# Kernel tuning notes

Hardware: AMD Instinct MI355X
Metric: run time of the kernel (lower is better)

Reference implementation:

```python
import jax, jax.numpy as jnp
import numpy as np

B, S, D, H, F, M, DC = 2, 1024, 1024, 16, 4096, 2048, 256
HD = D // H

def rmsnorm(x, w, eps=1e-6):
    return x * jax.lax.rsqrt(jnp.mean(x * x, axis=-1, keepdims=True) + eps) * w

def setup_inputs() -> dict:
    key = jax.random.key(0)
    ks = jax.random.split(key, 16)
    def w(i, shape):
        return jax.random.normal(ks[i], shape, jnp.float32) * (1.0 / np.sqrt(shape[0]))
    # real RoPE tables
    inv = 1.0 / (10000.0 ** (jnp.arange(0, HD, 2, dtype=jnp.float32) / HD))
    freqs = jnp.outer(jnp.arange(S, dtype=jnp.float32), inv)
    emb = jnp.concatenate([freqs, freqs], axis=-1)  # [S, HD]
    return {
        "hidden_states": jax.random.normal(ks[0], (B, S, D), jnp.float32),
        "mem_keys": jnp.zeros((B, M, DC), jnp.float32),
        "mem_values": jnp.zeros((B, M, D), jnp.float32),
        "cos": jnp.cos(emb), "sin": jnp.sin(emb),
        "norm1_w": jnp.ones((D,), jnp.float32),
        "norm2_w": jnp.ones((D,), jnp.float32),
        "norm_mem_w": jnp.ones((D,), jnp.float32),
        "Wq": w(1, (D, D)), "Wk": w(2, (D, D)), "Wv": w(3, (D, D)), "Wo": w(4, (D, D)),
        "W_content": w(5, (D, D)), "W_comp": w(6, (D, DC)), "W_strength": w(7, (D, 1)),
        "W_query": w(8, (D, DC)),
        "W_gate": w(9, (2 * D, D)), "W_proj": w(10, (D, D)),
        "W1": w(11, (D, F)), "W3": w(12, (D, F)), "W2": w(13, (F, D)),
        "position": 0,
    }

def reference(hidden_states, mem_keys, mem_values, cos, sin,
              norm1_w, norm2_w, norm_mem_w,
              Wq, Wk, Wv, Wo,
              W_content, W_comp, W_strength, W_query,
              W_gate, W_proj, W1, W3, W2, position):
    b, s, d = hidden_states.shape
    h = hidden_states
    # 1) causal self-attention with RoPE
    n = rmsnorm(h, norm1_w)
    def heads(x):
        return x.reshape(b, s, H, HD).transpose(0, 2, 1, 3)  # [b,h,s,hd]
    q, k, v = heads(n @ Wq), heads(n @ Wk), heads(n @ Wv)
    def rot(x):
        x1, x2 = jnp.split(x, 2, axis=-1)
        return jnp.concatenate([-x2, x1], axis=-1)
    c, si = cos[None, None], sin[None, None]
    q = q * c + rot(q) * si
    k = k * c + rot(k) * si
    scores = jnp.einsum('bhqd,bhkd->bhqk', q, k) / np.sqrt(HD)
    causal = jnp.tril(jnp.ones((s, s), bool))
    scores = jnp.where(causal, scores, jnp.float32(-1e30))
    attn = jax.nn.softmax(scores, axis=-1)
    attn_out = jnp.einsum('bhqk,bhkd->bhqd', attn, v).transpose(0, 2, 1, 3).reshape(b, s, d) @ Wo
    h = h + attn_out
    # 2) memory snapshot write: the original per-token python loop writes each token
    #    to consecutive circular-buffer slots; with M >= s the slots are unique, so
    #    the loop vectorizes into a single scatter.
    content = h @ W_content                     # [b,s,d]
    compressed = h @ W_comp                     # [b,s,DC]
    strength = jax.nn.sigmoid(h @ W_strength)   # [b,s,1]
    idx = (position + jnp.arange(s)) % mem_keys.shape[1]
    old_k = mem_keys[:, idx]
    old_v = mem_values[:, idx]
    new_keys = mem_keys.at[:, idx].set(strength * compressed + (1.0 - strength) * old_k)
    new_values = mem_values.at[:, idx].set(strength * content + (1.0 - strength) * old_v)
    # 3) memory retrieval (attention over slots)
    normed = rmsnorm(h, norm_mem_w)
    qm = normed @ W_query                       # [b,s,DC]
    mscores = jnp.einsum('bsd,bmd->bsm', qm, new_keys) / np.sqrt(DC)
    mattn = jax.nn.softmax(mscores, axis=-1)
    retrieved = jnp.einsum('bsm,bmd->bsd', mattn, new_values)
    # 4) gated memory integration
    gate = jax.nn.sigmoid(jnp.concatenate([h, retrieved], axis=-1) @ W_gate)
    h = h + gate * (retrieved @ W_proj)
    # 5) SwiGLU FFN
    n2 = rmsnorm(h, norm2_w)
    h = h + (jax.nn.silu(n2 @ W1) * (n2 @ W3)) @ W2
    return (h, new_keys, new_values)
```

## Files before the change

kernel.cpp:

```cpp
#include <hip/hip_runtime.h>
#include <hip/hip_bf16.h>
#include <math.h>

typedef __bf16 bf16;
typedef __attribute__((ext_vector_type(8))) __bf16 bf16x8;
typedef __attribute__((ext_vector_type(4))) __bf16 bf16x4;
typedef __attribute__((ext_vector_type(4))) float f32x4;

#define B_ 2
#define S_ 1024
#define D_ 1024
#define H_ 16
#define HD_ 64
#define F_ 4096
#define M_ 2048
#define DC_ 256
#define NTOK (B_*S_)

__device__ __forceinline__ void gload16(const void* g, void* l) {
    __builtin_amdgcn_global_load_lds(
        (__attribute__((address_space(1))) void*)(void*)(g),
        (__attribute__((address_space(3))) void*)(l), 16, 0, 0);
}

template<int N> __device__ __forceinline__ void wait_vm() {
    if constexpr (N == 0)      asm volatile("s_waitcnt vmcnt(0)" ::: "memory");
    else if constexpr (N == 2) asm volatile("s_waitcnt vmcnt(2)" ::: "memory");
    else if constexpr (N == 4) asm volatile("s_waitcnt vmcnt(4)" ::: "memory");
    else if constexpr (N == 6) asm volatile("s_waitcnt vmcnt(6)" ::: "memory");
    else                       asm volatile("s_waitcnt vmcnt(8)" ::: "memory");
}
__device__ __forceinline__ void wait_lgkm0() {
    asm volatile("s_waitcnt lgkmcnt(0)" ::: "memory");
}
__device__ __forceinline__ float sigm(float x) { return 1.f / (1.f + expf(-x)); }

template<int BM, int BN, bool OUTBF, int EPI>
__global__ __launch_bounds__(256) void mgemm(
    const bf16* __restrict__ A, const bf16* __restrict__ Bt,
    const float* __restrict__ resid, void* __restrict__ Cout,
    int K, int lda, int ldb, int ldc,
    long long sA, long long sB, long long sC,
    const void* __restrict__ aux1, const void* __restrict__ aux2)
{
    constexpr int WN   = (BM == 128) ? 2 : 4;
    constexpr int WCOL = BN / WN;
    constexpr int FN   = WCOL / 16;
    constexpr int LA = BM * 64, LB = BN * 64;
    constexpr int LPS = BM / 32 + BN / 32;
    __shared__ bf16 lds[2 * (LA + LB)];
    const int z = blockIdx.z;
    A  += (size_t)z * sA;
    Bt += (size_t)z * sB;
    const int gx = gridDim.x;
    const int nwg = gx * gridDim.y;
    const int flat = blockIdx.y * gx + blockIdx.x;
    const int q8 = nwg >> 3, r8 = nwg & 7;
    const int xcd = flat & 7, lid = flat >> 3;
    const int swz = (xcd < r8 ? xcd * (q8 + 1) : r8 * (q8 + 1) + (xcd - r8) * q8) + lid;
    const int band = swz / (8 * gx);
    const int rem  = swz % (8 * gx);
    const int row0 = (band * 8 + (rem & 7)) * BM;
    const int col0 = (rem >> 3) * BN;
    const int tid = threadIdx.x, wid = tid >> 6, lane = tid & 63;
    const int wr = wid / WN, wc = wid % WN;
    const int srow = lane >> 3;
    const int ssub = (lane & 7) ^ (srow & 7);

    f32x4 acc[4][FN];
    #pragma unroll
    for (int m = 0; m < 4; ++m)
        #pragma unroll
        for (int n = 0; n < FN; ++n) acc[m][n] = (f32x4){0.f, 0.f, 0.f, 0.f};

    auto STAGE = [&](int buf, int k0) {
        bf16* Ab = lds + buf * (LA + LB);
        bf16* Bb = Ab + LA;
        #pragma unroll
        for (int i = 0; i < BM / 32; ++i) {
            int c = wid * (BM / 32) + i;
            gload16(A + (size_t)(row0 + c * 8 + srow) * lda + k0 + ssub * 8, Ab + c * 512);
        }
        #pragma unroll
        for (int i = 0; i < BN / 32; ++i) {
            int c = wid * (BN / 32) + i;
            gload16(Bt + (size_t)(col0 + c * 8 + srow) * ldb + k0 + ssub * 8, Bb + c * 512);
        }
    };

    const int nt = K >> 6;
    STAGE(0, 0);
    if (nt > 1) STAGE(1, 64);
    for (int t = 0; t < nt; ++t) {
        if (t < nt - 1) wait_vm<LPS>();
        else            wait_vm<0>();
        __builtin_amdgcn_sched_barrier(0);
        __builtin_amdgcn_s_barrier();
        __builtin_amdgcn_sched_barrier(0);
        const bf16* Ab = lds + (t & 1) * (LA + LB);
        const bf16* Bb = Ab + LA;
        const int ar = wr * 64 + (lane & 15);
        const int br = wc * WCOL + (lane & 15);
        #pragma unroll
        for (int ksel = 0; ksel < 2; ++ksel) {
            const int ps = ((ksel << 2) + (lane >> 4)) ^ (lane & 7);
            bf16x8 af[4], bfr[FN];
            #pragma unroll
            for (int m = 0; m < 4; ++m)
                af[m] = *(const bf16x8*)(Ab + (ar + m * 16) * 64 + ps * 8);
            #pragma unroll
            for (int n = 0; n < FN; ++n)
                bfr[n] = *(const bf16x8*)(Bb + (br + n * 16) * 64 + ps * 8);
            #pragma unroll
            for (int m = 0; m < 4; ++m)
                #pragma unroll
                for (int n = 0; n < FN; ++n)
                    acc[m][n] = __builtin_amdgcn_mfma_f32_16x16x32_bf16(af[m], bfr[n], acc[m][n], 0, 0, 0);
        }
        wait_lgkm0();
        __builtin_amdgcn_sched_barrier(0);
        __builtin_amdgcn_s_barrier();
        __builtin_amdgcn_sched_barrier(0);
        if (t + 2 < nt) STAGE(t & 1, (t + 2) << 6);
    }
    const int crow = row0 + wr * 64 + ((lane >> 4) << 2);
    const int ccol = col0 + wc * WCOL + (lane & 15);
    #pragma unroll
    for (int m = 0; m < 4; ++m)
        #pragma unroll
        for (int n = 0; n < FN; ++n)
            #pragma unroll
            for (int r = 0; r < 4; ++r) {
                const int rr = crow + m * 16 + r, cc = ccol + n * 16;
                size_t idx = (size_t)rr * ldc + cc;
                float v = acc[m][n][r];
                if (EPI == 2) {
                    float g = sigm((float)((const bf16*)aux1)[idx]);
                    v = ((const float*)aux2)[idx] + g * v;
                    ((float*)Cout)[idx] = v;
                } else {
                    if (resid) v += resid[idx];
                    if (OUTBF) ((bf16*)Cout)[(size_t)z * sC + idx] = (bf16)v;
                    else       ((float*)Cout)[(size_t)z * sC + idx] = v;
                    if (EPI == 1)
                        ((bf16*)aux1)[(size_t)rr * 2048 + cc] = (bf16)v;
                }
            }
}

__global__ __launch_bounds__(256) void mgemm13(
    const bf16* __restrict__ A, const bf16* __restrict__ B1t, const bf16* __restrict__ B3t,
    bf16* __restrict__ Cout, int K, int lda, int ldb, int ldc)
{
    constexpr int LA = 128 * 64, LB = 64 * 64;
    __shared__ bf16 lds[2 * (LA + 2 * LB)];
    const int gx = gridDim.x;
    const int nwg = gx * gridDim.y;
    const int flat = blockIdx.y * gx + blockIdx.x;
    const int q8 = nwg >> 3, r8 = nwg & 7;
    const int xcd = flat & 7, lid = flat >> 3;
    const int swz = (xcd < r8 ? xcd * (q8 + 1) : r8 * (q8 + 1) + (xcd - r8) * q8) + lid;
    const int band = swz / (8 * gx);
    const int rem  = swz % (8 * gx);
    const int row0 = (band * 8 + (rem & 7)) * 128;
    const int col0 = (rem >> 3) * 64;
    const int tid = threadIdx.x, wid = tid >> 6, lane = tid & 63;
    const int wr = wid >> 1, wc = wid & 1;
    const int srow = lane >> 3;
    const int ssub = (lane & 7) ^ (srow & 7);

    f32x4 acc1[4][2], acc3[4][2];
    #pragma unroll
    for (int m = 0; m < 4; ++m)
        #pragma unroll
        for (int n = 0; n < 2; ++n) {
            acc1[m][n] = (f32x4){0.f, 0.f, 0.f, 0.f};
            acc3[m][n] = (f32x4){0.f, 0.f, 0.f, 0.f};
        }

    auto STAGE = [&](int buf, int k0) {
        bf16* Ab = lds + buf * (LA + 2 * LB);
        bf16* B1b = Ab + LA;
        bf16* B3b = B1b + LB;
        #pragma unroll
        for (int i = 0; i < 4; ++i) {
            int c = wid * 4 + i;
            gload16(A + (size_t)(row0 + c * 8 + srow) * lda + k0 + ssub * 8, Ab + c * 512);
        }
        #pragma unroll
        for (int i = 0; i < 2; ++i) {
            int c = wid * 2 + i;
            gload16(B1t + (size_t)(col0 + c * 8 + srow) * ldb + k0 + ssub * 8, B1b + c * 512);
            gload16(B3t + (size_t)(col0 + c * 8 + srow) * ldb + k0 + ssub * 8, B3b + c * 512);
        }
    };

    const int nt = K >> 6;
    STAGE(0, 0);
    if (nt > 1) STAGE(1, 64);
    for (int t = 0; t < nt; ++t) {
        if (t < nt - 1) wait_vm<8>();
        else            wait_vm<0>();
        __builtin_amdgcn_sched_barrier(0);
        __builtin_amdgcn_s_barrier();
        __builtin_amdgcn_sched_barrier(0);
        const bf16* Ab = lds + (t & 1) * (LA + 2 * LB);
        const bf16* B1b = Ab + LA;
        const bf16* B3b = B1b + LB;
        const int ar = wr * 64 + (lane & 15);
        const int br = wc * 32 + (lane & 15);
        #pragma unroll
        for (int ksel = 0; ksel < 2; ++ksel) {
            const int ps = ((ksel << 2) + (lane >> 4)) ^ (lane & 7);
            bf16x8 af[4], b1f[2], b3f[2];
            #pragma unroll
            for (int m = 0; m < 4; ++m)
                af[m] = *(const bf16x8*)(Ab + (ar + m * 16) * 64 + ps * 8);
            #pragma unroll
            for (int n = 0; n < 2; ++n) {
                b1f[n] = *(const bf16x8*)(B1b + (br + n * 16) * 64 + ps * 8);
                b3f[n] = *(const bf16x8*)(B3b + (br + n * 16) * 64 + ps * 8);
            }
            #pragma unroll
            for (int m = 0; m < 4; ++m)
                #pragma unroll
                for (int n = 0; n < 2; ++n) {
                    acc1[m][n] = __builtin_amdgcn_mfma_f32_16x16x32_bf16(af[m], b1f[n], acc1[m][n], 0, 0, 0);
                    acc3[m][n] = __builtin_amdgcn_mfma_f32_16x16x32_bf16(af[m], b3f[n], acc3[m][n], 0, 0, 0);
                }
        }
        wait_lgkm0();
        __builtin_amdgcn_sched_barrier(0);
        __builtin_amdgcn_s_barrier();
        __builtin_amdgcn_sched_barrier(0);
        if (t + 2 < nt) STAGE(t & 1, (t + 2) << 6);
    }
    const int crow = row0 + wr * 64 + ((lane >> 4) << 2);
    const int ccol = col0 + wc * 32 + (lane & 15);
    #pragma unroll
    for (int m = 0; m < 4; ++m)
        #pragma unroll
        for (int n = 0; n < 2; ++n)
            #pragma unroll
            for (int r = 0; r < 4; ++r) {
                float x = acc1[m][n][r];
                float v = (x * sigm(x)) * acc3[m][n][r];
                Cout[(size_t)(crow + m * 16 + r) * ldc + ccol + n * 16] = (bf16)v;
            }
}

__global__ __launch_bounds__(256) void flash_attn(
    const bf16* __restrict__ qkv, const bf16* __restrict__ vt,
    bf16* __restrict__ o)
{
    __shared__ bf16 qlds[64 * 64];
    __shared__ bf16 klds[2][64 * 64];
    __shared__ bf16 vlds[2][64 * 64];
    __shared__ bf16 plds[4][16 * 64];
    const int qt = blockIdx.x, hh = blockIdx.y, b = blockIdx.z;
    const int qb0 = qt * 64;
    const int tid = threadIdx.x, wid = tid >> 6, lane = tid & 63;
    const bf16* qg = qkv + (size_t)b * S_ * 3072 + hh * 64;
    const bf16* kg = qg + 1024;
    const bf16* vg = vt + (size_t)(b * H_ + hh) * 64 * 1024;
    const int srow = lane >> 3;
    const int ssub = (lane & 7) ^ (srow & 7);

    #pragma unroll
    for (int i = 0; i < 2; ++i) {
        int c = wid * 2 + i;
        gload16(qg + (size_t)(qb0 + c * 8 + srow) * 3072 + ssub * 8, qlds + c * 512);
    }
    auto STAGE = [&](int buf, int kb) {
        #pragma unroll
        for (int i = 0; i < 2; ++i) {
            int c = wid * 2 + i;
            gload16(kg + (size_t)(kb + c * 8 + srow) * 3072 + ssub * 8, klds[buf] + c * 512);
            gload16(vg + (size_t)(c * 8 + srow) * 1024 + kb + ssub * 8, vlds[buf] + c * 512);
        }
    };

    const int nt = qt + 1;
    STAGE(0, 0);
    if (nt > 1) STAGE(1, 64);

    f32x4 oacc[4];
    #pragma unroll
    for (int n = 0; n < 4; ++n) oacc[n] = (f32x4){0.f, 0.f, 0.f, 0.f};
    float mrow[4] = {-1e30f, -1e30f, -1e30f, -1e30f};
    float lrow[4] = {0.f, 0.f, 0.f, 0.f};
    bf16x8 qf[2];
    bf16* pw = plds[wid];
    const int qlr = (lane >> 4) * 4;

    for (int t = 0; t < nt; ++t) {
        if (t < nt - 1) wait_vm<4>();
        else            wait_vm<0>();
        __builtin_amdgcn_sched_barrier(0);
        __builtin_amdgcn_s_barrier();
        __builtin_amdgcn_sched_barrier(0);
        if (t == 0) {
            const int ar = wid * 16 + (lane & 15);
            #pragma unroll
            for (int ksel = 0; ksel < 2; ++ksel) {
                const int ps = ((ksel << 2) + (lane >> 4)) ^ (lane & 7);
                qf[ksel] = *(const bf16x8*)(qlds + ar * 64 + ps * 8);
            }
        }
        const bf16* Kb = klds[t & 1];
        const bf16* Vb = vlds[t & 1];
        f32x4 sacc[4];
        #pragma unroll
        for (int n = 0; n < 4; ++n) sacc[n] = (f32x4){0.f, 0.f, 0.f, 0.f};
        #pragma unroll
        for (int ksel = 0; ksel < 2; ++ksel) {
            const int ps = ((ksel << 2) + (lane >> 4)) ^ (lane & 7);
            #pragma unroll
            for (int n = 0; n < 4; ++n) {
                bf16x8 kf = *(const bf16x8*)(Kb + (n * 16 + (lane & 15)) * 64 + ps * 8);
                sacc[n] = __builtin_amdgcn_mfma_f32_16x16x32_bf16(qf[ksel], kf, sacc[n], 0, 0, 0);
            }
        }
        if (t == nt - 1) {
            const int qrow = qb0 + wid * 16 + qlr;
            const int kcol = t * 64 + (lane & 15);
            #pragma unroll
            for (int n = 0; n < 4; ++n)
                #pragma unroll
                for (int r = 0; r < 4; ++r)
                    if (kcol + n * 16 > qrow + r) sacc[n][r] = -1e30f;
        }
        #pragma unroll
        for (int r = 0; r < 4; ++r) {
            float mx = fmaxf(fmaxf(sacc[0][r], sacc[1][r]), fmaxf(sacc[2][r], sacc[3][r]));
            #pragma unroll
            for (int off = 8; off > 0; off >>= 1) mx = fmaxf(mx, __shfl_xor(mx, off));
            float mnew = fmaxf(mrow[r], mx);
            float scale = __expf(mrow[r] - mnew);
            float rs = 0.f;
            #pragma unroll
            for (int n = 0; n < 4; ++n) {
                float p = __expf(sacc[n][r] - mnew);
                sacc[n][r] = p;
                rs += p;
            }
            #pragma unroll
            for (int off = 8; off > 0; off >>= 1) rs += __shfl_xor(rs, off);
            lrow[r] = lrow[r] * scale + rs;
            mrow[r] = mnew;
            #pragma unroll
            for (int n = 0; n < 4; ++n) oacc[n][r] *= scale;
        }
        #pragma unroll
        for (int n = 0; n < 4; ++n)
            #pragma unroll
            for (int r = 0; r < 4; ++r) {
                const int qr = qlr + r;
                const int k = n * 16 + (lane & 15);
                const int su = (k >> 3) ^ (qr & 7);
                pw[qr * 64 + su * 8 + (k & 7)] = (bf16)sacc[n][r];
            }
        #pragma unroll
        for (int ksel = 0; ksel < 2; ++ksel) {
            const int ps = ((ksel << 2) + (lane >> 4)) ^ (lane & 7);
            bf16x8 pa = *(const bf16x8*)(pw + (lane & 15) * 64 + ps * 8);
            #pragma unroll
            for (int n = 0; n < 4; ++n) {
                bf16x8 vf = *(const bf16x8*)(Vb + (n * 16 + (lane & 15)) * 64 + ps * 8);
                oacc[n] = __builtin_amdgcn_mfma_f32_16x16x32_bf16(pa, vf, oacc[n], 0, 0, 0);
            }
        }
        wait_lgkm0();
        __builtin_amdgcn_sched_barrier(0);
        __builtin_amdgcn_s_barrier();
        __builtin_amdgcn_sched_barrier(0);
        if (t + 2 < nt) STAGE(t & 1, (t + 2) * 64);
    }
    float inv[4];
    #pragma unroll
    for (int r = 0; r < 4; ++r) inv[r] = 1.f / lrow[r];
    #pragma unroll
    for (int n = 0; n < 4; ++n)
        #pragma unroll
        for (int r = 0; r < 4; ++r) {
            const int q = qb0 + wid * 16 + qlr + r;
            const int d = n * 16 + (lane & 15);
            o[(size_t)(b * S_ + q) * 1024 + hh * 64 + d] = (bf16)(oacc[n][r] * inv[r]);
        }
}

template<typename TI>
__global__ __launch_bounds__(256) void tcast(
    const TI* __restrict__ in, bf16* __restrict__ out,
    int lin, int lout, long long sin, long long sout)
{
    __shared__ float t[32][33];
    in  += (size_t)blockIdx.z * sin;
    out += (size_t)blockIdx.z * sout;
    const int c0 = blockIdx.x * 32, r0 = blockIdx.y * 32;
    const int tx = threadIdx.x & 31, ty = threadIdx.x >> 5;
    #pragma unroll
    for (int j = 0; j < 4; ++j)
        t[ty + j * 8][tx] = (float)in[(size_t)(r0 + ty + j * 8) * lin + c0 + tx];
    __syncthreads();
    #pragma unroll
    for (int j = 0; j < 4; ++j)
        out[(size_t)(c0 + ty + j * 8) * lout + r0 + tx] = (bf16)t[tx][ty + j * 8];
}

struct TC6 { const float* in[6]; bf16* out[6]; };
__global__ __launch_bounds__(256) void tcast_b(TC6 p, int lin, int lout)
{
    __shared__ float t[32][33];
    const float* in = p.in[blockIdx.z];
    bf16* out = p.out[blockIdx.z];
    const int c0 = blockIdx.x * 32, r0 = blockIdx.y * 32;
    const int tx = threadIdx.x & 31, ty = threadIdx.x >> 5;
    #pragma unroll
    for (int j = 0; j < 4; ++j)
        t[ty + j * 8][tx] = in[(size_t)(r0 + ty + j * 8) * lin + c0 + tx];
    __syncthreads();
    #pragma unroll
    for (int j = 0; j < 4; ++j)
        out[(size_t)(c0 + ty + j * 8) * lout + r0 + tx] = (bf16)t[tx][ty + j * 8];
}

__global__ __launch_bounds__(256) void rmsnorm_bf(
    const float* __restrict__ x, const float* __restrict__ w, bf16* __restrict__ out)
{
    __shared__ float red[4];
    const int row = blockIdx.x, tid = threadIdx.x;
    const float* xr = x + (size_t)row * D_;
    f32x4 v = *(const f32x4*)(xr + tid * 4);
    float ss = v.x * v.x + v.y * v.y + v.z * v.z + v.w * v.w;
    #pragma unroll
    for (int off = 32; off > 0; off >>= 1) ss += __shfl_xor(ss, off);
    if ((tid & 63) == 0) red[tid >> 6] = ss;
    __syncthreads();
    float scn = rsqrtf((red[0] + red[1] + red[2] + red[3]) * (1.f / D_) + 1e-6f);
    f32x4 wv = *(const f32x4*)(w + tid * 4);
    bf16x4 o;
    o[0] = (bf16)(v.x * scn * wv.x); o[1] = (bf16)(v.y * scn * wv.y);
    o[2] = (bf16)(v.z * scn * wv.z); o[3] = (bf16)(v.w * scn * wv.w);
    *(bf16x4*)(out + (size_t)row * D_ + tid * 4) = o;
}

__global__ __launch_bounds__(256) void h1_post(
    const float* __restrict__ h1, const float* __restrict__ nmw,
    const float* __restrict__ wst, bf16* __restrict__ nbf, float* __restrict__ stb)
{
    __shared__ float red[4], red2[4];
    const int row = blockIdx.x, tid = threadIdx.x;
    const float* xr = h1 + (size_t)row * D_;
    f32x4 v = *(const f32x4*)(xr + tid * 4);
    f32x4 wv = *(const f32x4*)(wst + tid * 4);
    float ss = v.x * v.x + v.y * v.y + v.z * v.z + v.w * v.w;
    float dt = v.x * wv.x + v.y * wv.y + v.z * wv.z + v.w * wv.w;
    #pragma unroll
    for (int off = 32; off > 0; off >>= 1) {
        ss += __shfl_xor(ss, off);
        dt += __shfl_xor(dt, off);
    }
    if ((tid & 63) == 0) { red[tid >> 6] = ss; red2[tid >> 6] = dt; }
    __syncthreads();
    float scn = rsqrtf((red[0] + red[1] + red[2] + red[3]) * (1.f / D_) + 1e-6f);
    f32x4 nw = *(const f32x4*)(nmw + tid * 4);
    bf16x4 o;
    o[0] = (bf16)(v.x * scn * nw.x); o[1] = (bf16)(v.y * scn * nw.y);
    o[2] = (bf16)(v.z * scn * nw.z); o[3] = (bf16)(v.w * scn * nw.w);
    *(bf16x4*)(nbf + (size_t)row * D_ + tid * 4) = o;
    if (tid == 0) stb[row] = sigm(red2[0] + red2[1] + red2[2] + red2[3]);
}

__global__ __launch_bounds__(256) void rope_vt(
    bf16* __restrict__ qkv, const float* __restrict__ cosp,
    const float* __restrict__ sinp, bf16* __restrict__ vt)
{
    __shared__ bf16 vl[64][72];
    const int st = blockIdx.x, hh = blockIdx.y, b = blockIdx.z;
    const int tid = threadIdx.x;
    const int r = tid >> 2;
    const int p0 = (tid & 3) * 8;
    const int s = st * 64 + r;
    bf16* base = qkv + ((size_t)(b * S_ + s)) * 3072 + hh * 64;
    {
        f32x4 c1a = *(const f32x4*)(cosp + s * 64 + p0);
        f32x4 c1b = *(const f32x4*)(cosp + s * 64 + p0 + 4);
        f32x4 s1a = *(const f32x4*)(sinp + s * 64 + p0);
        f32x4 s1b = *(const f32x4*)(sinp + s * 64 + p0 + 4);
        f32x4 c2a = *(const f32x4*)(cosp + s * 64 + p0 + 32);
        f32x4 c2b = *(const f32x4*)(cosp + s * 64 + p0 + 36);
        f32x4 s2a = *(const f32x4*)(sinp + s * 64 + p0 + 32);
        f32x4 s2b = *(const f32x4*)(sinp + s * 64 + p0 + 36);
        float c1[8] = {c1a.x,c1a.y,c1a.z,c1a.w,c1b.x,c1b.y,c1b.z,c1b.w};
        float s1[8] = {s1a.x,s1a.y,s1a.z,s1a.w,s1b.x,s1b.y,s1b.z,s1b.w};
        float c2[8] = {c2a.x,c2a.y,c2a.z,c2a.w,c2b.x,c2b.y,c2b.z,c2b.w};
        float s2[8] = {s2a.x,s2a.y,s2a.z,s2a.w,s2b.x,s2b.y,s2b.z,s2b.w};
        #pragma unroll
        for (int which = 0; which < 2; ++which) {
            bf16* ptr = base + which * 1024;
            bf16x8 x1 = *(const bf16x8*)(ptr + p0);
            bf16x8 x2 = *(const bf16x8*)(ptr + p0 + 32);
            bf16x8 o1, o2;
            float qs = which ? 1.f : 0.125f;
            #pragma unroll
            for (int j = 0; j < 8; ++j) {
                float a = (float)x1[j], bb = (float)x2[j];
                o1[j] = (bf16)((a * c1[j] - bb * s1[j]) * qs);
                o2[j] = (bf16)((bb * c2[j] + a * s2[j]) * qs);
            }
            *(bf16x8*)(ptr + p0) = o1;
            *(bf16x8*)(ptr + p0 + 32) = o2;
        }
    }
    {
        const int d0 = (tid & 3) * 16;
        bf16x8 v0 = *(const bf16x8*)(base + 2048 + d0);
        bf16x8 v1 = *(const bf16x8*)(base + 2048 + d0 + 8);
        #pragma unroll
        for (int j = 0; j < 8; ++j) { vl[r][d0 + j] = v0[j]; vl[r][d0 + 8 + j] = v1[j]; }
    }
    __syncthreads();
    {
        const int d = tid >> 2;
        const int sq = (tid & 3) * 16;
        bf16x8 o0, o1;
        #pragma unroll
        for (int j = 0; j < 8; ++j) { o0[j] = vl[sq + j][d]; o1[j] = vl[sq + 8 + j][d]; }
        bf16* dst = vt + (size_t)(b * H_ + hh) * 65536 + (size_t)d * 1024 + st * 64 + sq;
        *(bf16x8*)(dst) = o0;
        *(bf16x8*)(dst + 8) = o1;
    }
}

__global__ __launch_bounds__(256) void mem_softmax(
    const bf16* __restrict__ ms, bf16* __restrict__ out)
{
    __shared__ float red[4];
    const int row = blockIdx.x, tid = threadIdx.x;
    bf16x8 iv = *(const bf16x8*)(ms + (size_t)row * 2048 + tid * 8);
    float xs[8];
    float mx = -1e30f;
    #pragma unroll
    for (int i = 0; i < 8; ++i) { xs[i] = (float)iv[i]; mx = fmaxf(mx, xs[i]); }
    #pragma unroll
    for (int off = 32; off > 0; off >>= 1) mx = fmaxf(mx, __shfl_xor(mx, off));
    if ((tid & 63) == 0) red[tid >> 6] = mx;
    __syncthreads();
    mx = fmaxf(fmaxf(red[0], red[1]), fmaxf(red[2], red[3]));
    __syncthreads();
    float sum = 0.f;
    #pragma unroll
    for (int i = 0; i < 8; ++i) { xs[i] = __expf((xs[i] - mx) * 0.0625f); sum += xs[i]; }
    #pragma unroll
    for (int off = 32; off > 0; off >>= 1) sum += __shfl_xor(sum, off);
    if ((tid & 63) == 0) red[tid >> 6] = sum;
    __syncthreads();
    float inv = 1.f / (red[0] + red[1] + red[2] + red[3]);
    bf16x8 o;
    #pragma unroll
    for (int i = 0; i < 8; ++i) o[i] = (bf16)(xs[i] * inv);
    *(bf16x8*)(out + (size_t)row * 2048 + tid * 8) = o;
}

__global__ void mem_upd(const float* __restrict__ ctcp, const float* __restrict__ st,
                        const float* __restrict__ memk, const float* __restrict__ memv,
                        const int* __restrict__ pos,
                        float* __restrict__ outk, float* __restrict__ outv,
                        bf16* __restrict__ okbf)
{
    int idx = blockIdx.x * 256 + threadIdx.x;
    const int NV = B_ * M_ * D_ / 4;
    if (idx < NV) {
        int c = (idx & 255) * 4;
        int row = (idx >> 8) & (M_ - 1);
        int b = idx >> 19;
        int s = (row - pos[0]) % M_; if (s < 0) s += M_;
        size_t mi = ((size_t)b * M_ + row) * D_ + c;
        f32x4 o = *(const f32x4*)(memv + mi);
        if (s < S_) {
            float t = st[b * S_ + s];
            f32x4 cv = *(const f32x4*)(ctcp + ((size_t)b * S_ + s) * 1280 + c);
            o.x = t * cv.x + (1.f - t) * o.x; o.y = t * cv.y + (1.f - t) * o.y;
            o.z = t * cv.z + (1.f - t) * o.z; o.w = t * cv.w + (1.f - t) * o.w;
        }
        *(f32x4*)(outv + mi) = o;
    } else {
        idx -= NV;
        int c = (idx & 63) * 4;
        int row = (idx >> 6) & (M_ - 1);
        int b = idx >> 17;
        int s = (row - pos[0]) % M_; if (s < 0) s += M_;
        size_t mi = ((size_t)b * M_ + row) * DC_ + c;
        f32x4 o = *(const f32x4*)(memk + mi);
        if (s < S_) {
            float t = st[b * S_ + s];
            f32x4 cv = *(const f32x4*)(ctcp + ((size_t)b * S_ + s) * 1280 + 1024 + c);
            o.x = t * cv.x + (1.f - t) * o.x; o.y = t * cv.y + (1.f - t) * o.y;
            o.z = t * cv.z + (1.f - t) * o.z; o.w = t * cv.w + (1.f - t) * o.w;
        }
        *(f32x4*)(outk + mi) = o;
        bf16x4 ob = {(bf16)o.x, (bf16)o.y, (bf16)o.z, (bf16)o.w};
        *(bf16x4*)(okbf + mi) = ob;
    }
}

extern "C" void kernel_launch(void* const* d_in, const int* in_sizes, int n_in,
                              void* d_out, int out_size, void* d_ws, size_t ws_size,
                              hipStream_t stream)
{
    const float* h0   = (const float*)d_in[0];
    const float* memk = (const float*)d_in[1];
    const float* memv = (const float*)d_in[2];
    const float* cosp = (const float*)d_in[3];
    const float* sinp = (const float*)d_in[4];
    const float* n1w  = (const float*)d_in[5];
    const float* n2w  = (const float*)d_in[6];
    const float* nmw  = (const float*)d_in[7];
    const float* Wq   = (const float*)d_in[8];
    const float* Wk   = (const float*)d_in[9];
    const float* Wv   = (const float*)d_in[10];
    const float* Wo   = (const float*)d_in[11];
    const float* Wct  = (const float*)d_in[12];
    const float* Wcp  = (const float*)d_in[13];
    const float* Wst  = (const float*)d_in[14];
    const float* Wqr  = (const float*)d_in[15];
    const float* Wg   = (const float*)d_in[16];
    const float* Wpj  = (const float*)d_in[17];
    const float* W1   = (const float*)d_in[18];
    const float* W3   = (const float*)d_in[19];
    const float* W2   = (const float*)d_in[20];
    const int*   pos  = (const int*)d_in[21];

    float* out_h = (float*)d_out;
    float* out_k = out_h + (size_t)NTOK * D_;
    float* out_v = out_k + (size_t)B_ * M_ * DC_;

    char* W = (char*)d_ws;
    const size_t MB = 1u << 20;
    bf16*  qkvb = (bf16*)(W);
    bf16*  vtb  = (bf16*)(W + 12 * MB);
    bf16*  nbf  = (bf16*)(W + 16 * MB);
    bf16*  abf  = (bf16*)(W + 20 * MB);
    float* h1b  = (float*)(W + 24 * MB);
    bf16*  catbf= (bf16*)(W + 32 * MB);
    float* ctcp = (float*)(W + 40 * MB);
    float* stb  = (float*)(W + 51 * MB);
    bf16*  msbf = (bf16*)(W + 52 * MB);
    bf16*  matt = (bf16*)(W + 68 * MB);
    bf16*  nvt  = (bf16*)(W + 76 * MB);
    bf16*  a1bf = (bf16*)(W);
    bf16*  okbf = (bf16*)(W + 84 * MB);
    bf16*  qmbf = (bf16*)(W + 86 * MB);
    bf16*  aobf = (bf16*)(W + 88 * MB);
    float* h2b  = (float*)(W + 96 * MB);
    bf16*  WqkvT= (bf16*)(W + 104 * MB);
    bf16*  WoT  = (bf16*)(W + 110 * MB);
    bf16*  WctcpT=(bf16*)(W + 112 * MB);
    bf16*  WqrT = (bf16*)(W + 115 * MB);
    bf16*  WgT  = (bf16*)(W + 116 * MB);
    bf16*  WpjT = (bf16*)(W + 120 * MB);
    bf16*  W13T = (bf16*)(W + 122 * MB);
    bf16*  W2T  = (bf16*)(W + 138 * MB);

    {
        TC6 pa;
        pa.in[0] = Wq;  pa.out[0] = WqkvT;
        pa.in[1] = Wk;  pa.out[1] = WqkvT + 1024 * 1024;
        pa.in[2] = Wv;  pa.out[2] = WqkvT + 2048 * 1024;
        pa.in[3] = Wo;  pa.out[3] = WoT;
        pa.in[4] = Wct; pa.out[4] = WctcpT;
        pa.in[5] = Wpj; pa.out[5] = WpjT;
        tcast_b<<<dim3(32, 32, 6), 256, 0, stream>>>(pa, 1024, 1024);
        TC6 pb;
        pb.in[0] = Wcp; pb.out[0] = WctcpT + 1024 * 1024;
        pb.in[1] = Wqr; pb.out[1] = WqrT;
        pb.in[2] = Wcp; pb.out[2] = WctcpT + 1024 * 1024;
        pb.in[3] = Wcp; pb.out[3] = WctcpT + 1024 * 1024;
        pb.in[4] = Wcp; pb.out[4] = WctcpT + 1024 * 1024;
        pb.in[5] = Wcp; pb.out[5] = WctcpT + 1024 * 1024;
        tcast_b<<<dim3(8, 32, 2), 256, 0, stream>>>(pb, 256, 1024);
        TC6 pc;
        pc.in[0] = W1; pc.out[0] = W13T;
        pc.in[1] = W3; pc.out[1] = W13T + 4096 * 1024;
        pc.in[2] = W1; pc.out[2] = W13T;
        pc.in[3] = W1; pc.out[3] = W13T;
        pc.in[4] = W1; pc.out[4] = W13T;
        pc.in[5] = W1; pc.out[5] = W13T;
        tcast_b<<<dim3(128, 32, 2), 256, 0, stream>>>(pc, 4096, 1024);
    }
    tcast<float><<<dim3(32, 64, 1), 256, 0, stream>>>(Wg, WgT, 1024, 2048, 0, 0);
    tcast<float><<<dim3(32, 128, 1), 256, 0, stream>>>(W2, W2T, 1024, 4096, 0, 0);

    rmsnorm_bf<<<NTOK, 256, 0, stream>>>(h0, n1w, nbf);
    mgemm<64, 128, true, 0><<<dim3(24, 32, 1), 256, 0, stream>>>(
        nbf, WqkvT, nullptr, qkvb, 1024, 1024, 1024, 3072, 0, 0, 0, nullptr, nullptr);
    rope_vt<<<dim3(S_ / 64, H_, B_), 256, 0, stream>>>(qkvb, cosp, sinp, vtb);

    flash_attn<<<dim3(S_ / 64, H_, B_), 256, 0, stream>>>(qkvb, vtb, abf);

    mgemm<64, 64, false, 1><<<dim3(16, 32, 1), 256, 0, stream>>>(
        abf, WoT, h0, h1b, 1024, 1024, 1024, 1024, 0, 0, 0, catbf, nullptr);
    h1_post<<<NTOK, 256, 0, stream>>>(h1b, nmw, Wst, nbf, stb);

    mgemm<64, 64, false, 0><<<dim3(20, 32, 1), 256, 0, stream>>>(
        catbf, WctcpT, nullptr, ctcp, 1024, 2048, 1024, 1280, 0, 0, 0, nullptr, nullptr);
    mem_upd<<<(B_ * M_ * D_ / 4 + B_ * M_ * DC_ / 4) / 256, 256, 0, stream>>>(
        ctcp, stb, memk, memv, pos, out_k, out_v, okbf);

    mgemm<64, 64, true, 0><<<dim3(4, 32, 1), 256, 0, stream>>>(
        nbf, WqrT, nullptr, qmbf, 1024, 1024, 1024, 256, 0, 0, 0, nullptr, nullptr);
    mgemm<64, 128, true, 0><<<dim3(16, 16, 2), 256, 0, stream>>>(
        qmbf, okbf, nullptr, msbf, 256, 256, 256, 2048,
        (long long)S_ * 256, (long long)M_ * 256, (long long)S_ * 2048, nullptr, nullptr);
    mem_softmax<<<NTOK, 256, 0, stream>>>(msbf, matt);
    tcast<float><<<dim3(32, 64, 2), 256, 0, stream>>>(
        out_v, nvt, 1024, 2048, (long long)M_ * 1024, (long long)1024 * 2048);
    mgemm<64, 128, true, 0><<<dim3(8, 16, 2), 256, 0, stream>>>(
        matt, nvt, nullptr, catbf + 1024, 2048, 2048, 2048, 2048,
        (long long)S_ * 2048, (long long)1024 * 2048, (long long)S_ * 2048, nullptr, nullptr);

    mgemm<64, 64, true, 0><<<dim3(16, 32, 1), 256, 0, stream>>>(
        catbf, WgT, nullptr, aobf, 2048, 2048, 2048, 1024, 0, 0, 0, nullptr, nullptr);
    mgemm<64, 64, false, 2><<<dim3(16, 32, 1), 256, 0, stream>>>(
        catbf + 1024, WpjT, nullptr, h2b, 1024, 2048, 1024, 1024, 0, 0, 0, aobf, h1b);

    rmsnorm_bf<<<NTOK, 256, 0, stream>>>(h2b, n2w, nbf);
    mgemm13<<<dim3(64, 16, 1), 256, 0, stream>>>(
        nbf, W13T, W13T + 4096 * 1024, a1bf, 1024, 1024, 1024, 4096);
    mgemm<64, 64, false, 0><<<dim3(16, 32, 1), 256, 0, stream>>>(
        a1bf, W2T, h2b, out_h, 4096, 4096, 4096, 1024, 0, 0, 0, nullptr, nullptr);
}
```

Measured before the change: 284.3 us.

## Fuse gate and projection GEMMs, merge weight transposes, fold value transpose into memory update

Several changes land together. The separate gate GEMM and projection GEMM become one kernel that accumulates both products and applies the sigmoid-gated residual in the epilogue, so the bf16 gate intermediate no longer goes through memory. All weight transpose/cast launches collapse into a single flat-grid kernel, removing launch overhead. The content/compression GEMM now writes bf16 instead of fp32, and the memory update writes the transposed bf16 values directly, dropping the separate transpose pass over out_v. The bf16 intermediate lowers the precision of the updated memory contents.

```diff
diff --git a/kernel.cpp b/kernel.cpp
--- a/kernel.cpp
+++ b/kernel.cpp
@@ -41,7 +41,7 @@
     const float* __restrict__ resid, void* __restrict__ Cout,
     int K, int lda, int ldb, int ldc,
     long long sA, long long sB, long long sC,
-    const void* __restrict__ aux1, const void* __restrict__ aux2)
+    void* __restrict__ aux1)
 {
     constexpr int WN   = (BM == 128) ? 2 : 4;
     constexpr int WCOL = BN / WN;
@@ -134,18 +134,113 @@
                 const int rr = crow + m * 16 + r, cc = ccol + n * 16;
                 size_t idx = (size_t)rr * ldc + cc;
                 float v = acc[m][n][r];
-                if (EPI == 2) {
-                    float g = sigm((float)((const bf16*)aux1)[idx]);
-                    v = ((const float*)aux2)[idx] + g * v;
-                    ((float*)Cout)[idx] = v;
-                } else {
-                    if (resid) v += resid[idx];
-                    if (OUTBF) ((bf16*)Cout)[(size_t)z * sC + idx] = (bf16)v;
-                    else       ((float*)Cout)[(size_t)z * sC + idx] = v;
-                    if (EPI == 1)
-                        ((bf16*)aux1)[(size_t)rr * 2048 + cc] = (bf16)v;
-                }
-            }
+                if (resid) v += resid[idx];
+                if (OUTBF) ((bf16*)Cout)[(size_t)z * sC + idx] = (bf16)v;
+                else       ((float*)Cout)[(size_t)z * sC + idx] = v;
+                if (EPI == 1)
+                    ((bf16*)aux1)[(size_t)rr * 2048 + cc] = (bf16)v;
+            }
+}
+
+__global__ __launch_bounds__(256) void mgemm_gp(
+    const bf16* __restrict__ A, const bf16* __restrict__ B1t, const bf16* __restrict__ B3t,
+    const float* __restrict__ h1, float* __restrict__ h2)
+{
+    constexpr int LA = 64 * 64, LB = 64 * 64;
+    __shared__ bf16 lds[2 * (LA + 2 * LB)];
+    const int gx = gridDim.x;
+    const int nwg = gx * gridDim.y;
+    const int flat = blockIdx.y * gx + blockIdx.x;
+    const int q8 = nwg >> 3, r8 = nwg & 7;
+    const int xcd = flat & 7, lid = flat >> 3;
+    const int swz = (xcd < r8 ? xcd * (q8 + 1) : r8 * (q8 + 1) + (xcd - r8) * q8) + lid;
+    const int band = swz / (8 * gx);
+    const int rem  = swz % (8 * gx);
+    const int row0 = (band * 8 + (rem & 7)) * 64;
+    const int col0 = (rem >> 3) * 64;
+    const int tid = threadIdx.x, wid = tid >> 6, lane = tid & 63;
+    const int wc = wid;
+    const int srow = lane >> 3;
+    const int ssub = (lane & 7) ^ (srow & 7);
+
+    f32x4 acc1[4], acc3[4];
+    #pragma unroll
+    for (int m = 0; m < 4; ++m) {
+        acc1[m] = (f32x4){0.f, 0.f, 0.f, 0.f};
+        acc3[m] = (f32x4){0.f, 0.f, 0.f, 0.f};
+    }
+
+    auto STAGE = [&](int buf, int tt) {
+        bf16* Ab = lds + buf * (LA + 2 * LB);
+        bf16* B1b = Ab + LA;
+        bf16* B3b = B1b + LB;
+        const int k0 = tt << 6;
+        #pragma unroll
+        for (int i = 0; i < 2; ++i) {
+            int c = wid * 2 + i;
+            gload16(A + (size_t)(row0 + c * 8 + srow) * 2048 + k0 + ssub * 8, Ab + c * 512);
+        }
+        #pragma unroll
+        for (int i = 0; i < 2; ++i) {
+            int c = wid * 2 + i;
+            gload16(B1t + (size_t)(col0 + c * 8 + srow) * 2048 + k0 + ssub * 8, B1b + c * 512);
+        }
+        if (tt >= 16) {
+            const int k3 = (tt - 16) << 6;
+            #pragma unroll
+            for (int i = 0; i < 2; ++i) {
+                int c = wid * 2 + i;
+                gload16(B3t + (size_t)(col0 + c * 8 + srow) * 1024 + k3 + ssub * 8, B3b + c * 512);
+            }
+        }
+    };
+
+    STAGE(0, 0);
+    STAGE(1, 1);
+    for (int t = 0; t < 32; ++t) {
+        if (t < 31) { if (t + 1 >= 16) wait_vm<6>(); else wait_vm<4>(); }
+        else wait_vm<0>();
+        __builtin_amdgcn_sched_barrier(0);
+        __builtin_amdgcn_s_barrier();
+        __builtin_amdgcn_sched_barrier(0);
+        const bf16* Ab = lds + (t & 1) * (LA + 2 * LB);
+        const bf16* B1b = Ab + LA;
+        const bf16* B3b = B1b + LB;
+        const int ar = lane & 15;
+        const int br = wc * 16 + (lane & 15);
+        #pragma unroll
+        for (int ksel = 0; ksel < 2; ++ksel) {
+            const int ps = ((ksel << 2) + (lane >> 4)) ^ (lane & 7);
+            bf16x8 af[4], b1f, b3f;
+            #pragma unroll
+            for (int m = 0; m < 4; ++m)
+                af[m] = *(const bf16x8*)(Ab + (ar + m * 16) * 64 + ps * 8);
+            b1f = *(const bf16x8*)(B1b + br * 64 + ps * 8);
+            #pragma unroll
+            for (int m = 0; m < 4; ++m)
+                acc1[m] = __builtin_amdgcn_mfma_f32_16x16x32_bf16(af[m], b1f, acc1[m], 0, 0, 0);
+            if (t >= 16) {
+                b3f = *(const bf16x8*)(B3b + br * 64 + ps * 8);
+                #pragma unroll
+                for (int m = 0; m < 4; ++m)
+                    acc3[m] = __builtin_amdgcn_mfma_f32_16x16x32_bf16(af[m], b3f, acc3[m], 0, 0, 0);
+            }
+        }
+        wait_lgkm0();
+        __builtin_amdgcn_sched_barrier(0);
+        __builtin_amdgcn_s_barrier();
+        __builtin_amdgcn_sched_barrier(0);
+        if (t + 2 < 32) STAGE(t & 1, t + 2);
+    }
+    const int crow = row0 + ((lane >> 4) << 2);
+    const int ccol = col0 + wc * 16 + (lane & 15);
+    #pragma unroll
+    for (int m = 0; m < 4; ++m)
+        #pragma unroll
+        for (int r = 0; r < 4; ++r) {
+            size_t idx = (size_t)(crow + m * 16 + r) * 1024 + ccol;
+            h2[idx] = h1[idx] + sigm(acc1[m][r]) * acc3[m][r];
+        }
 }
 
 __global__ __launch_bounds__(256) void mgemm13(
@@ -389,40 +484,28 @@
         }
 }
 
-template<typename TI>
-__global__ __launch_bounds__(256) void tcast(
-    const TI* __restrict__ in, bf16* __restrict__ out,
-    int lin, int lout, long long sin, long long sout)
+struct TCD { const float* src; bf16* dst; int ct; int rt; int start; };
+struct TCA { TCD e[12]; };
+__global__ __launch_bounds__(256) void tcast_all(TCA p)
 {
     __shared__ float t[32][33];
-    in  += (size_t)blockIdx.z * sin;
-    out += (size_t)blockIdx.z * sout;
-    const int c0 = blockIdx.x * 32, r0 = blockIdx.y * 32;
+    const int flat = blockIdx.x;
+    int i = 0;
+    #pragma unroll
+    for (int j = 1; j < 12; ++j) if (flat >= p.e[j].start) i = j;
+    const TCD d = p.e[i];
+    const int local = flat - d.start;
+    const int cx = local % d.ct, ry = local / d.ct;
+    const int C = d.ct * 32, R = d.rt * 32;
+    const int c0 = cx * 32, r0 = ry * 32;
     const int tx = threadIdx.x & 31, ty = threadIdx.x >> 5;
     #pragma unroll
     for (int j = 0; j < 4; ++j)
-        t[ty + j * 8][tx] = (float)in[(size_t)(r0 + ty + j * 8) * lin + c0 + tx];
+        t[ty + j * 8][tx] = d.src[(size_t)(r0 + ty + j * 8) * C + c0 + tx];
     __syncthreads();
     #pragma unroll
     for (int j = 0; j < 4; ++j)
-        out[(size_t)(c0 + ty + j * 8) * lout + r0 + tx] = (bf16)t[tx][ty + j * 8];
-}
-
-struct TC6 { const float* in[6]; bf16* out[6]; };
-__global__ __launch_bounds__(256) void tcast_b(TC6 p, int lin, int lout)
-{
-    __shared__ float t[32][33];
-    const float* in = p.in[blockIdx.z];
-    bf16* out = p.out[blockIdx.z];
-    const int c0 = blockIdx.x * 32, r0 = blockIdx.y * 32;
-    const int tx = threadIdx.x & 31, ty = threadIdx.x >> 5;
-    #pragma unroll
-    for (int j = 0; j < 4; ++j)
-        t[ty + j * 8][tx] = in[(size_t)(r0 + ty + j * 8) * lin + c0 + tx];
-    __syncthreads();
-    #pragma unroll
-    for (int j = 0; j < 4; ++j)
-        out[(size_t)(c0 + ty + j * 8) * lout + r0 + tx] = (bf16)t[tx][ty + j * 8];
+        d.dst[(size_t)(c0 + ty + j * 8) * R + r0 + tx] = (bf16)t[tx][ty + j * 8];
 }
 
 __global__ __launch_bounds__(256) void rmsnorm_bf(
@@ -563,45 +646,86 @@
     *(bf16x8*)(out + (size_t)row * 2048 + tid * 8) = o;
 }
 
-__global__ void mem_upd(const float* __restrict__ ctcp, const float* __restrict__ st,
-                        const float* __restrict__ memk, const float* __restrict__ memv,
-                        const int* __restrict__ pos,
-                        float* __restrict__ outk, float* __restrict__ outv,
-                        bf16* __restrict__ okbf)
-{
-    int idx = blockIdx.x * 256 + threadIdx.x;
-    const int NV = B_ * M_ * D_ / 4;
-    if (idx < NV) {
-        int c = (idx & 255) * 4;
-        int row = (idx >> 8) & (M_ - 1);
-        int b = idx >> 19;
-        int s = (row - pos[0]) % M_; if (s < 0) s += M_;
-        size_t mi = ((size_t)b * M_ + row) * D_ + c;
-        f32x4 o = *(const f32x4*)(memv + mi);
-        if (s < S_) {
-            float t = st[b * S_ + s];
-            f32x4 cv = *(const f32x4*)(ctcp + ((size_t)b * S_ + s) * 1280 + c);
-            o.x = t * cv.x + (1.f - t) * o.x; o.y = t * cv.y + (1.f - t) * o.y;
-            o.z = t * cv.z + (1.f - t) * o.z; o.w = t * cv.w + (1.f - t) * o.w;
-        }
-        *(f32x4*)(outv + mi) = o;
+__global__ __launch_bounds__(256) void mem_upd2(
+    const bf16* __restrict__ ctcp, const float* __restrict__ st,
+    const float* __restrict__ memk, const float* __restrict__ memv,
+    const int* __restrict__ pos,
+    float* __restrict__ outk, float* __restrict__ outv,
+    bf16* __restrict__ okbf, bf16* __restrict__ nvt)
+{
+    __shared__ float tl[64][65];
+    const int dt = blockIdx.x, mt = blockIdx.y, b = blockIdx.z;
+    const int tid = threadIdx.x;
+    const int r = tid >> 2, q = tid & 3;
+    const int m = mt * 64 + r;
+    int s = (m - pos[0]) % M_; if (s < 0) s += M_;
+    const bool upd = (s < S_);
+    const float t = upd ? st[b * S_ + s] : 0.f;
+    float res[16];
+    if (dt < 16) {
+        const int c0 = dt * 64 + q * 16;
+        size_t vi = ((size_t)b * M_ + m) * D_ + c0;
+        #pragma unroll
+        for (int j = 0; j < 4; ++j) {
+            f32x4 o = *(const f32x4*)(memv + vi + j * 4);
+            res[4*j] = o.x; res[4*j+1] = o.y; res[4*j+2] = o.z; res[4*j+3] = o.w;
+        }
+        if (upd) {
+            const bf16* cp = ctcp + ((size_t)(b * S_ + s)) * 1280 + c0;
+            bf16x8 ca = *(const bf16x8*)cp;
+            bf16x8 cb = *(const bf16x8*)(cp + 8);
+            #pragma unroll
+            for (int j = 0; j < 8; ++j) {
+                res[j]     = t * (float)ca[j] + (1.f - t) * res[j];
+                res[8 + j] = t * (float)cb[j] + (1.f - t) * res[8 + j];
+            }
+        }
+        #pragma unroll
+        for (int j = 0; j < 4; ++j) {
+            f32x4 o = {res[4*j], res[4*j+1], res[4*j+2], res[4*j+3]};
+            *(f32x4*)(outv + vi + j * 4) = o;
+        }
+        #pragma unroll
+        for (int j = 0; j < 16; ++j) tl[r][q * 16 + j] = res[j];
+        __syncthreads();
+        const int rd = tid >> 2;
+        bf16x8 oa, ob;
+        #pragma unroll
+        for (int j = 0; j < 8; ++j) {
+            oa[j] = (bf16)tl[q * 16 + j][rd];
+            ob[j] = (bf16)tl[q * 16 + 8 + j][rd];
+        }
+        bf16* dst = nvt + (size_t)b * 1024 * 2048 + (size_t)(dt * 64 + rd) * 2048 + mt * 64 + q * 16;
+        *(bf16x8*)dst = oa;
+        *(bf16x8*)(dst + 8) = ob;
     } else {
-        idx -= NV;
-        int c = (idx & 63) * 4;
-        int row = (idx >> 6) & (M_ - 1);
-        int b = idx >> 17;
-        int s = (row - pos[0]) % M_; if (s < 0) s += M_;
-        size_t mi = ((size_t)b * M_ + row) * DC_ + c;
-        f32x4 o = *(const f32x4*)(memk + mi);
-        if (s < S_) {
-            float t = st[b * S_ + s];
-            f32x4 cv = *(const f32x4*)(ctcp + ((size_t)b * S_ + s) * 1280 + 1024 + c);
-            o.x = t * cv.x + (1.f - t) * o.x; o.y = t * cv.y + (1.f - t) * o.y;
-            o.z = t * cv.z + (1.f - t) * o.z; o.w = t * cv.w + (1.f - t) * o.w;
-        }
-        *(f32x4*)(outk + mi) = o;
-        bf16x4 ob = {(bf16)o.x, (bf16)o.y, (bf16)o.z, (bf16)o.w};
-        *(bf16x4*)(okbf + mi) = ob;
+        const int c0 = (dt - 16) * 64 + q * 16;
+        size_t ki = ((size_t)b * M_ + m) * DC_ + c0;
+        #pragma unroll
+        for (int j = 0; j < 4; ++j) {
+            f32x4 o = *(const f32x4*)(memk + ki + j * 4);
+            res[4*j] = o.x; res[4*j+1] = o.y; res[4*j+2] = o.z; res[4*j+3] = o.w;
+        }
+        if (upd) {
+            const bf16* cp = ctcp + ((size_t)(b * S_ + s)) * 1280 + 1024 + c0;
+            bf16x8 ca = *(const bf16x8*)cp;
+            bf16x8 cb = *(const bf16x8*)(cp + 8);
+            #pragma unroll
+            for (int j = 0; j < 8; ++j) {
+                res[j]     = t * (float)ca[j] + (1.f - t) * res[j];
+                res[8 + j] = t * (float)cb[j] + (1.f - t) * res[8 + j];
+            }
+        }
+        bf16x8 oa, ob;
+        #pragma unroll
+        for (int j = 0; j < 4; ++j) {
+            f32x4 o = {res[4*j], res[4*j+1], res[4*j+2], res[4*j+3]};
+            *(f32x4*)(outk + ki + j * 4) = o;
+        }
+        #pragma unroll
+        for (int j = 0; j < 8; ++j) { oa[j] = (bf16)res[j]; ob[j] = (bf16)res[8 + j]; }
+        *(bf16x8*)(okbf + ki) = oa;
+        *(bf16x8*)(okbf + ki + 8) = ob;
     }
 }
 
@@ -644,7 +768,7 @@
     bf16*  abf  = (bf16*)(W + 20 * MB);
     float* h1b  = (float*)(W + 24 * MB);
     bf16*  catbf= (bf16*)(W + 32 * MB);
-    float* ctcp = (float*)(W + 40 * MB);
+    bf16*  ctcp = (bf16*)(W + 40 * MB);
     float* stb  = (float*)(W + 51 * MB);
     bf16*  msbf = (bf16*)(W + 52 * MB);
     bf16*  matt = (bf16*)(W + 68 * MB);
@@ -652,7 +776,6 @@
     bf16*  a1bf = (bf16*)(W);
     bf16*  okbf = (bf16*)(W + 84 * MB);
     bf16*  qmbf = (bf16*)(W + 86 * MB);
-    bf16*  aobf = (bf16*)(W + 88 * MB);
     float* h2b  = (float*)(W + 96 * MB);
     bf16*  WqkvT= (bf16*)(W + 104 * MB);
     bf16*  WoT  = (bf16*)(W + 110 * MB);
@@ -664,70 +787,57 @@
     bf16*  W2T  = (bf16*)(W + 138 * MB);
 
     {
-        TC6 pa;
-        pa.in[0] = Wq;  pa.out[0] = WqkvT;
-        pa.in[1] = Wk;  pa.out[1] = WqkvT + 1024 * 1024;
-        pa.in[2] = Wv;  pa.out[2] = WqkvT + 2048 * 1024;
-        pa.in[3] = Wo;  pa.out[3] = WoT;
-        pa.in[4] = Wct; pa.out[4] = WctcpT;
-        pa.in[5] = Wpj; pa.out[5] = WpjT;
-        tcast_b<<<dim3(32, 32, 6), 256, 0, stream>>>(pa, 1024, 1024);
-        TC6 pb;
-        pb.in[0] = Wcp; pb.out[0] = WctcpT + 1024 * 1024;
-        pb.in[1] = Wqr; pb.out[1] = WqrT;
-        pb.in[2] = Wcp; pb.out[2] = WctcpT + 1024 * 1024;
-        pb.in[3] = Wcp; pb.out[3] = WctcpT + 1024 * 1024;
-        pb.in[4] = Wcp; pb.out[4] = WctcpT + 1024 * 1024;
-        pb.in[5] = Wcp; pb.out[5] = WctcpT + 1024 * 1024;
-        tcast_b<<<dim3(8, 32, 2), 256, 0, stream>>>(pb, 256, 1024);
-        TC6 pc;
-        pc.in[0] = W1; pc.out[0] = W13T;
-        pc.in[1] = W3; pc.out[1] = W13T + 4096 * 1024;
-        pc.in[2] = W1; pc.out[2] = W13T;
-        pc.in[3] = W1; pc.out[3] = W13T;
-        pc.in[4] = W1; pc.out[4] = W13T;
-        pc.in[5] = W1; pc.out[5] = W13T;
-        tcast_b<<<dim3(128, 32, 2), 256, 0, stream>>>(pc, 4096, 1024);
-    }
-    tcast<float><<<dim3(32, 64, 1), 256, 0, stream>>>(Wg, WgT, 1024, 2048, 0, 0);
-    tcast<float><<<dim3(32, 128, 1), 256, 0, stream>>>(W2, W2T, 1024, 4096, 0, 0);
+        TCA p;
+        auto set = [&](int i, const float* s, bf16* d, int ct, int rt, int st_) {
+            p.e[i].src = s; p.e[i].dst = d; p.e[i].ct = ct; p.e[i].rt = rt; p.e[i].start = st_;
+        };
+        int off = 0;
+        set(0,  Wq,  WqkvT,               32, 32,  off); off += 1024;
+        set(1,  Wk,  WqkvT + 1024 * 1024, 32, 32,  off); off += 1024;
+        set(2,  Wv,  WqkvT + 2048 * 1024, 32, 32,  off); off += 1024;
+        set(3,  Wo,  WoT,                 32, 32,  off); off += 1024;
+        set(4,  Wct, WctcpT,              32, 32,  off); off += 1024;
+        set(5,  Wpj, WpjT,                32, 32,  off); off += 1024;
+        set(6,  Wcp, WctcpT + 1024 * 1024, 8, 32,  off); off += 256;
+        set(7,  Wqr, WqrT,                 8, 32,  off); off += 256;
+        set(8,  Wg,  WgT,                 32, 64,  off); off += 2048;
+        set(9,  W1,  W13T,               128, 32,  off); off += 4096;
+        set(10, W3,  W13T + 4096 * 1024, 128, 32,  off); off += 4096;
+        set(11, W2,  W2T,                 32, 128, off); off += 4096;
+        tcast_all<<<off, 256, 0, stream>>>(p);
+    }
 
     rmsnorm_bf<<<NTOK, 256, 0, stream>>>(h0, n1w, nbf);
     mgemm<64, 128, true, 0><<<dim3(24, 32, 1), 256, 0, stream>>>(
-        nbf, WqkvT, nullptr, qkvb, 1024, 1024, 1024, 3072, 0, 0, 0, nullptr, nullptr);
+        nbf, WqkvT, nullptr, qkvb, 1024, 1024, 1024, 3072, 0, 0, 0, nullptr);
     rope_vt<<<dim3(S_ / 64, H_, B_), 256, 0, stream>>>(qkvb, cosp, sinp, vtb);
 
     flash_attn<<<dim3(S_ / 64, H_, B_), 256, 0, stream>>>(qkvb, vtb, abf);
 
     mgemm<64, 64, false, 1><<<dim3(16, 32, 1), 256, 0, stream>>>(
-        abf, WoT, h0, h1b, 1024, 1024, 1024, 1024, 0, 0, 0, catbf, nullptr);
+        abf, WoT, h0, h1b, 1024, 1024, 1024, 1024, 0, 0, 0, catbf);
     h1_post<<<NTOK, 256, 0, stream>>>(h1b, nmw, Wst, nbf, stb);
 
-    mgemm<64, 64, false, 0><<<dim3(20, 32, 1), 256, 0, stream>>>(
-        catbf, WctcpT, nullptr, ctcp, 1024, 2048, 1024, 1280, 0, 0, 0, nullptr, nullptr);
-    mem_upd<<<(B_ * M_ * D_ / 4 + B_ * M_ * DC_ / 4) / 256, 256, 0, stream>>>(
-        ctcp, stb, memk, memv, pos, out_k, out_v, okbf);
+    mgemm<64, 64, true, 0><<<dim3(20, 32, 1), 256, 0, stream>>>(
+        catbf, WctcpT, nullptr, ctcp, 1024, 2048, 1024, 1280, 0, 0, 0, nullptr);
+    mem_upd2<<<dim3(20, 32, 2), 256, 0, stream>>>(
+        ctcp, stb, memk, memv, pos, out_k, out_v, okbf, nvt);
 
     mgemm<64, 64, true, 0><<<dim3(4, 32, 1), 256, 0, stream>>>(
-        nbf, WqrT, nullptr, qmbf, 1024, 1024, 1024, 256, 0, 0, 0, nullptr, nullptr);
+        nbf, WqrT, nullptr, qmbf, 1024, 1024, 1024, 256, 0, 0, 0, nullptr);
     mgemm<64, 128, true, 0><<<dim3(16, 16, 2), 256, 0, stream>>>(
         qmbf, okbf, nullptr, msbf, 256, 256, 256, 2048,
-        (long long)S_ * 256, (long long)M_ * 256, (long long)S_ * 2048, nullptr, nullptr);
+        (long long)S_ * 256, (long long)M_ * 256, (long long)S_ * 2048, nullptr);
     mem_softmax<<<NTOK, 256, 0, stream>>>(msbf, matt);
-    tcast<float><<<dim3(32, 64, 2), 256, 0, stream>>>(
-        out_v, nvt, 1024, 2048, (long long)M_ * 1024, (long long)1024 * 2048);
     mgemm<64, 128, true, 0><<<dim3(8, 16, 2), 256, 0, stream>>>(
         matt, nvt, nullptr, catbf + 1024, 2048, 2048, 2048, 2048,
-        (long long)S_ * 2048, (long long)1024 * 2048, (long long)S_ * 2048, nullptr, nullptr);
-
-    mgemm<64, 64, true, 0><<<dim3(16, 32, 1), 256, 0, stream>>>(
-        catbf, WgT, nullptr, aobf, 2048, 2048, 2048, 1024, 0, 0, 0, nullptr, nullptr);
-    mgemm<64, 64, false, 2><<<dim3(16, 32, 1), 256, 0, stream>>>(
-        catbf + 1024, WpjT, nullptr, h2b, 1024, 2048, 1024, 1024, 0, 0, 0, aobf, h1b);
+        (long long)S_ * 2048, (long long)1024 * 2048, (long long)S_ * 2048, nullptr);
+
+    mgemm_gp<<<dim3(16, 32, 1), 256, 0, stream>>>(catbf, WgT, WpjT, h1b, h2b);
 
     rmsnorm_bf<<<NTOK, 256, 0, stream>>>(h2b, n2w, nbf);
     mgemm13<<<dim3(64, 16, 1), 256, 0, stream>>>(
         nbf, W13T, W13T + 4096 * 1024, a1bf, 1024, 1024, 1024, 4096);
     mgemm<64, 64, false, 0><<<dim3(16, 32, 1), 256, 0, stream>>>(
-        a1bf, W2T, h2b, out_h, 4096, 4096, 4096, 1024, 0, 0, 0, nullptr, nullptr);
-}
+        a1bf, W2T, h2b, out_h, 4096, 4096, 4096, 1024, 0, 0, 0, nullptr);
+}
```

After: 275.1 us. 3.2% less time.
